# Performance work log

Hardware: AMD Instinct MI355X
Metric: run time of the kernel (lower is better)

## Reference

```python
import jax, jax.numpy as jnp
import numpy as np

HEADS = 8

def _conv1x1(x, W, b):
    # x: [n, Cin, H, W]; W: [Cout, Cin]; b: [Cout]
    return jnp.einsum('nchw,oc->nohw', x, W) + b[None, :, None, None]

def setup_inputs() -> dict:
    key = jax.random.key(0)
    ks = jax.random.split(key, 11)
    n, Cin, H, W = 8, 256, 80, 80
    Ck, Cv = 256, 256
    s_in = 1.0 / np.sqrt(Cin)
    s_v = 1.0 / np.sqrt(Cv)
    return {
        'query_feature': jax.random.normal(ks[0], (n, Cin, H, W), jnp.float32),
        'key_feature': jax.random.normal(ks[1], (n, Cin, H, W), jnp.float32),
        'value_feature': jax.random.normal(ks[2], (n, Cin, H, W), jnp.float32),
        'Wq': jax.random.normal(ks[3], (Ck, Cin), jnp.float32) * s_in,
        'bq': jax.random.normal(ks[4], (Ck,), jnp.float32) * s_in,
        'Wk': jax.random.normal(ks[5], (Ck, Cin), jnp.float32) * s_in,
        'bk': jax.random.normal(ks[6], (Ck,), jnp.float32) * s_in,
        'Wv': jax.random.normal(ks[7], (Cv, Cin), jnp.float32) * s_in,
        'bv': jax.random.normal(ks[8], (Cv,), jnp.float32) * s_in,
        'Wr': jax.random.normal(ks[9], (Cin, Cv), jnp.float32) * s_v,
        'br': jax.random.normal(ks[10], (Cin,), jnp.float32) * s_v,
    }

def reference(query_feature, key_feature, value_feature, Wq, bq, Wk, bk, Wv, bv, Wr, br):
    n, _, qh, qw = query_feature.shape
    kvn, _, kvh, kvw = key_feature.shape
    Ck = Wq.shape[0]
    Cv = Wv.shape[0]
    hk = Ck // HEADS
    hv = Cv // HEADS
    Lq = qh * qw
    Lkv = kvh * kvw
    # 1x1 conv projections, split channels into heads (consecutive channel blocks)
    q = _conv1x1(query_feature, Wq, bq).reshape(n, HEADS, hk, Lq)
    k = _conv1x1(key_feature, Wk, bk).reshape(kvn, HEADS, hk, Lkv)
    v = _conv1x1(value_feature, Wv, bv).reshape(kvn, HEADS, hv, Lkv)
    # softmax: keys over spatial positions, queries over head channels
    k = jax.nn.softmax(k, axis=3)
    q = jax.nn.softmax(q, axis=2)
    # efficient (linear) attention: context = K @ V^T, out = context^T @ Q
    context = jnp.einsum('nhkl,nhvl->nhkv', k, v)          # [n, H, hk, hv]
    attended = jnp.einsum('nhkv,nhkl->nhvl', context, q)   # [n, H, hv, Lq]
    aggregated = attended.reshape(n, Cv, qh, qw)
    return _conv1x1(aggregated, Wr, br) + query_feature
```

## Files before the change

### kernel.cpp

```cpp
#include <hip/hip_runtime.h>
#include <hip/hip_bf16.h>

#define NB 8
#define C 256
#define LL 6400
#define HEADS 8
#define HC 32
#define NH 64
#define SEG 40
#define SL 160
#define QPP 264
#define XTP 264

typedef unsigned short u16;
typedef unsigned int u32;
typedef __attribute__((ext_vector_type(8))) short bf16x8;
typedef __attribute__((ext_vector_type(4))) float f32x4;

typedef __attribute__((address_space(1))) const u32 ga_u32;
typedef __attribute__((address_space(3))) u32 ls_u32;

__device__ __forceinline__ void gload_lds16(const u16* g, u16* l) {
  __builtin_amdgcn_global_load_lds((ga_u32*)g, (ls_u32*)l, 16, 0, 0);
}

__device__ __forceinline__ float bf2f(u32 u) { return __uint_as_float(u << 16); }
__device__ __forceinline__ u16 f2bf(float f) {
  __hip_bfloat16 h = __float2bfloat16(f);
  return *(u16*)&h;
}
__device__ __forceinline__ void unpack8(uint4 u, float* f) {
  f[0] = bf2f(u.x & 0xffffu); f[1] = bf2f(u.x >> 16);
  f[2] = bf2f(u.y & 0xffffu); f[3] = bf2f(u.y >> 16);
  f[4] = bf2f(u.z & 0xffffu); f[5] = bf2f(u.z >> 16);
  f[6] = bf2f(u.w & 0xffffu); f[7] = bf2f(u.w >> 16);
}

struct WcvtArgs { const float* W[3]; u16* Wb[3]; };
struct PFArgs { const float* X[3]; const u16* Wb[3]; const float* bias[3]; u16* P[3]; };

__global__ __launch_bounds__(256) void wcvt(WcvtArgs a) {
  const int idx = blockIdx.x * 256 + threadIdx.x;
  const int which = idx >> 14, off = (idx & 16383) * 4;
  float4 v = *(const float4*)&a.W[which][off];
  ushort4 o = {f2bf(v.x), f2bf(v.y), f2bf(v.z), f2bf(v.w)};
  *(ushort4*)&a.Wb[which][off] = o;
}

__global__ __launch_bounds__(256, 2) void proj_fused(PFArgs args) {
  __shared__ __align__(16) u16 Xt[64 * XTP];
  __shared__ __align__(16) u16 Bs[2][256 * 32];
  const int which = blockIdx.y >> 3, n = blockIdx.y & 7;
  const int l0 = blockIdx.x * 64;
  const int t = threadIdx.x;
  const int lane = t & 63, wave = t >> 6;
  const int fr = lane & 15, q = lane >> 4;
  const int wl = (wave & 1) * 32, wco = (wave >> 1) * 128;
  const int s16 = t & 15, rc16 = t >> 4;
  const int srow = t >> 2, scol = (t & 3) * 8;
  const float* X = args.X[which] + (size_t)n * C * LL;
  const u16* Wb = args.Wb[which];

#pragma unroll
  for (int s = 0; s < 4; ++s)
    gload_lds16(&Wb[(size_t)(s * 64 + srow) * C + scol], &Bs[0][s * 2048 + wave * 512]);

  float4 xv[16];
#pragma unroll
  for (int cc = 0; cc < 16; ++cc)
    xv[cc] = *(const float4*)&X[(size_t)(rc16 * 16 + cc) * LL + l0 + s16 * 4];
#pragma unroll
  for (int j = 0; j < 4; ++j) {
    const int l = s16 * 4 + j;
    u32 w[8];
#pragma unroll
    for (int p = 0; p < 8; ++p) {
      const float* e0 = (const float*)&xv[2 * p];
      const float* e1 = (const float*)&xv[2 * p + 1];
      w[p] = (u32)f2bf(e0[j]) | ((u32)f2bf(e1[j]) << 16);
    }
    const int base = l * XTP + rc16 * 16;
    const int sw = (l & 7) << 3;
    uint4 lo = {w[0], w[1], w[2], w[3]};
    uint4 hi = {w[4], w[5], w[6], w[7]};
    *(uint4*)&Xt[(base) ^ sw] = lo;
    *(uint4*)&Xt[(base + 8) ^ sw] = hi;
  }
  __syncthreads();

  f32x4 acc[2][8] = {};
#pragma unroll
  for (int kt = 0; kt < 8; ++kt) {
    if (kt < 7) {
#pragma unroll
      for (int s = 0; s < 4; ++s)
        gload_lds16(&Wb[(size_t)(s * 64 + srow) * C + (kt + 1) * 32 + scol],
                    &Bs[(kt + 1) & 1][s * 2048 + wave * 512]);
    }
    bf16x8 a[2];
#pragma unroll
    for (int i = 0; i < 2; ++i) {
      const int row = wl + i * 16 + fr;
      a[i] = *(const bf16x8*)&Xt[(row * XTP + kt * 32 + q * 8) ^ ((row & 7) << 3)];
    }
#pragma unroll
    for (int j = 0; j < 8; ++j) {
      bf16x8 b = *(const bf16x8*)&Bs[kt & 1][(wco + j * 16 + fr) * 32 + q * 8];
#pragma unroll
      for (int i = 0; i < 2; ++i)
        acc[i][j] = __builtin_amdgcn_mfma_f32_16x16x32_bf16(a[i], b, acc[i][j], 0, 0, 0);
    }
    __syncthreads();
  }

  const float* bias = args.bias[which];
  u16* P = args.P[which] + (size_t)n * LL * C;
  float bb[8];
#pragma unroll
  for (int j = 0; j < 8; ++j) bb[j] = bias[wco + j * 16 + fr];
#pragma unroll
  for (int i = 0; i < 2; ++i)
#pragma unroll
    for (int r = 0; r < 4; ++r) {
      const int lrow = wl + i * 16 + q * 4 + r;
#pragma unroll
      for (int j = 0; j < 8; ++j)
        Xt[lrow * XTP + wco + j * 16 + fr] = f2bf(acc[i][j][r] + bb[j]);
    }
  __syncthreads();
  const int rg = t >> 5, ch = t & 31;
#pragma unroll
  for (int s = 0; s < 8; ++s) {
    const int row = rg * 8 + s;
    bf16x8 vrow = *(const bf16x8*)&Xt[row * XTP + ch * 8];
    *(bf16x8*)&P[(size_t)(l0 + row) * C + ch * 8] = vrow;
  }
}

__global__ __launch_bounds__(256) void ctx_part(const u16* __restrict__ Kt,
    const u16* __restrict__ Vt, float* __restrict__ pctx, float* __restrict__ psum) {
  __shared__ __align__(16) u16 Ks[16 * 256];
  __shared__ __align__(16) u16 Vs[16 * 256];
  const int seg = blockIdx.x, n = blockIdx.y;
  const int t = threadIdx.x, lane = t & 63, wave = t >> 6;
  const int l0 = seg * SL;
  const u16* KtN = Kt + (size_t)n * LL * C;
  const u16* VtN = Vt + (size_t)n * LL * C;
  const int k4 = (lane & 7) * 4, v8 = lane >> 3;
  float acc[2][4][4] = {};
  float ssum[2][4] = {};
  for (int ls = 0; ls < SL; ls += 16) {
    __syncthreads();
#pragma unroll
    for (int i = 0; i < 2; ++i) {
      const int r = wave * 4 + i * 2;
      gload_lds16(&KtN[(size_t)(l0 + ls + r) * C + lane * 8], &Ks[r * 256]);
      gload_lds16(&VtN[(size_t)(l0 + ls + r) * C + lane * 8], &Vs[r * 256]);
    }
    __syncthreads();
#pragma unroll
    for (int hh = 0; hh < 2; ++hh) {
      const int h = wave * 2 + hh;
#pragma unroll
      for (int l = 0; l < 16; ++l) {
        ushort4 ku = *(const ushort4*)&Ks[l * 256 + h * 32 + k4];
        ushort4 vu = *(const ushort4*)&Vs[l * 256 + h * 32 + v8 * 4];
        float ek[4] = {__expf(bf2f(ku.x)), __expf(bf2f(ku.y)),
                       __expf(bf2f(ku.z)), __expf(bf2f(ku.w))};
        float vf[4] = {bf2f(vu.x), bf2f(vu.y), bf2f(vu.z), bf2f(vu.w)};
#pragma unroll
        for (int i = 0; i < 4; ++i)
#pragma unroll
          for (int j = 0; j < 4; ++j) acc[hh][i][j] = fmaf(ek[i], vf[j], acc[hh][i][j]);
        if (v8 == 0)
#pragma unroll
          for (int i = 0; i < 4; ++i) ssum[hh][i] += ek[i];
      }
    }
  }
#pragma unroll
  for (int hh = 0; hh < 2; ++hh) {
    const int h = wave * 2 + hh;
    const size_t pb = ((size_t)seg * NH + n * 8 + h) * 1024;
#pragma unroll
    for (int i = 0; i < 4; ++i)
#pragma unroll
      for (int j = 0; j < 4; ++j)
        pctx[pb + (size_t)(k4 + i) * 32 + v8 * 4 + j] = acc[hh][i][j];
    if (v8 == 0) {
      const size_t sb = ((size_t)seg * NH + n * 8 + h) * 32;
#pragma unroll
      for (int i = 0; i < 4; ++i) psum[sb + k4 + i] = ssum[hh][i];
    }
  }
}

__global__ __launch_bounds__(256) void ctx_reduce(const float* __restrict__ pctx,
    const float* __restrict__ psum, float* __restrict__ ctx) {
  const int idx = blockIdx.x * 256 + threadIdx.x;
  const int nh = idx >> 10, e = idx & 1023, k = e >> 5;
  float s = 0.f, ss = 0.f;
  for (int g = 0; g < SEG; ++g) {
    s += pctx[(size_t)(g * NH + nh) * 1024 + e];
    ss += psum[(size_t)(g * NH + nh) * 32 + k];
  }
  ctx[idx] = s / ss;
}

__global__ __launch_bounds__(256) void mfuse(const float* __restrict__ Wr,
    const float* __restrict__ ctx, u16* __restrict__ M) {
  const int idx = blockIdx.x * 256 + threadIdx.x;
  const int hk = idx & 255;
  const int o = (idx >> 8) & 255;
  const int n = idx >> 16;
  const int h = hk >> 5, k = hk & 31;
  const float* wr = Wr + (size_t)o * C + h * HC;
  const float* cx = ctx + ((size_t)(n * HEADS + h) * HC + k) * HC;
  float s = 0.f;
#pragma unroll
  for (int v = 0; v < HC; ++v) s = fmaf(wr[v], cx[v], s);
  M[idx] = f2bf(s);
}

__global__ __launch_bounds__(256) void out_fused(const u16* __restrict__ Qt,
    const u16* __restrict__ Mb, const float* __restrict__ br,
    const float* __restrict__ Xq, float* __restrict__ out) {
  __shared__ __align__(16) u16 Qp[64 * QPP];
  __shared__ __align__(16) u16 As[2][128 * 32];
  const int n = blockIdx.y, l0 = blockIdx.x * 64;
  const int t = threadIdx.x, lane = t & 63, wave = t >> 6;
  const int fr = lane & 15, q = lane >> 4;
  const int wcoL = (wave >> 1) * 64, wl = (wave & 1) * 32;
  const int srow = t >> 2, scol = (t & 3) * 8;
  const u16* QtN = Qt + (size_t)n * LL * C;
  const u16* MbN = Mb + (size_t)n * C * C;

#pragma unroll
  for (int s = 0; s < 2; ++s)
    gload_lds16(&MbN[(size_t)(s * 64 + srow) * C + scol], &As[0][s * 2048 + wave * 512]);

#pragma unroll
  for (int p = 0; p < 2; ++p) {
    const int row = p * 32 + (t >> 3);
    const int g = t & 7;
    const uint4* src = (const uint4*)&QtN[(size_t)(l0 + row) * C + g * 32];
    uint4 u0 = src[0], u1 = src[1], u2 = src[2], u3 = src[3];
    float v[32];
    unpack8(u0, v); unpack8(u1, v + 8); unpack8(u2, v + 16); unpack8(u3, v + 24);
    float e[32], s = 0.f;
#pragma unroll
    for (int j = 0; j < 32; ++j) { e[j] = __expf(v[j]); s += e[j]; }
    const float r = 1.0f / s;
    uint4* drow = (uint4*)&Qp[row * QPP + g * 32];
#pragma unroll
    for (int b4 = 0; b4 < 4; ++b4) {
      union { uint4 u; u16 h[8]; } o;
#pragma unroll
      for (int j = 0; j < 8; ++j) o.h[j] = f2bf(e[b4 * 8 + j] * r);
      drow[b4] = o.u;
    }
  }
  asm volatile("s_waitcnt vmcnt(0) lgkmcnt(0)" ::: "memory");
  __builtin_amdgcn_s_barrier();
  __builtin_amdgcn_sched_barrier(0);

  f32x4 acc[2][4][2] = {};
#pragma unroll
  for (int it = 0; it < 16; ++it) {
    const int coh = it >> 3, k0 = (it & 7) * 32, cur = it & 1;
    if (it < 15) {
      const int nco = (it + 1) >> 3, nk0 = ((it + 1) & 7) * 32;
#pragma unroll
      for (int s = 0; s < 2; ++s)
        gload_lds16(&MbN[(size_t)(nco * 128 + s * 64 + srow) * C + nk0 + scol],
                    &As[cur ^ 1][s * 2048 + wave * 512]);
      __builtin_amdgcn_sched_barrier(0);
    }
    bf16x8 a[4], b[2];
#pragma unroll
    for (int i = 0; i < 4; ++i)
      a[i] = *(const bf16x8*)&As[cur][(wcoL + i * 16 + fr) * 32 + q * 8];
#pragma unroll
    for (int j = 0; j < 2; ++j)
      b[j] = *(const bf16x8*)&Qp[(wl + j * 16 + fr) * QPP + k0 + q * 8];
#pragma unroll
    for (int i = 0; i < 4; ++i)
#pragma unroll
      for (int j = 0; j < 2; ++j)
        acc[coh][i][j] = __builtin_amdgcn_mfma_f32_16x16x32_bf16(a[i], b[j], acc[coh][i][j], 0, 0, 0);
    if (it < 15) {
      asm volatile("s_waitcnt vmcnt(0) lgkmcnt(0)" ::: "memory");
      __builtin_amdgcn_s_barrier();
      __builtin_amdgcn_sched_barrier(0);
    }
  }

  const float* XqN = Xq + (size_t)n * C * LL;
  float* On = out + (size_t)n * C * LL;
#pragma unroll
  for (int coh = 0; coh < 2; ++coh)
#pragma unroll
    for (int i = 0; i < 4; ++i)
#pragma unroll
      for (int r = 0; r < 4; ++r) {
        const int co = coh * 128 + wcoL + i * 16 + q * 4 + r;
        const float bb = br[co];
#pragma unroll
        for (int j = 0; j < 2; ++j) {
          const int l = l0 + wl + j * 16 + fr;
          const size_t off = (size_t)co * LL + l;
          On[off] = acc[coh][i][j][r] + bb + XqN[off];
        }
      }
}

extern "C" void kernel_launch(void* const* d_in, const int* in_sizes, int n_in,
                              void* d_out, int out_size, void* d_ws, size_t ws_size,
                              hipStream_t stream) {
  const float* Xq = (const float*)d_in[0];
  const float* Xk = (const float*)d_in[1];
  const float* Xv = (const float*)d_in[2];
  const float* Wq = (const float*)d_in[3];
  const float* bq = (const float*)d_in[4];
  const float* Wk = (const float*)d_in[5];
  const float* bk = (const float*)d_in[6];
  const float* Wv = (const float*)d_in[7];
  const float* bv = (const float*)d_in[8];
  const float* Wr = (const float*)d_in[9];
  const float* br = (const float*)d_in[10];
  float* out = (float*)d_out;

  char* ws = (char*)d_ws;
  const size_t nelem = (size_t)NB * LL * C;
  u16* Qt = (u16*)ws;
  u16* Kt = (u16*)(ws + nelem * 2);
  u16* Vt = (u16*)(ws + nelem * 4);
  char* p = ws + nelem * 6;
  u16* Wqb = (u16*)p; p += C * C * 2;
  u16* Wkb = (u16*)p; p += C * C * 2;
  u16* Wvb = (u16*)p; p += C * C * 2;
  float* pctx = (float*)p; p += (size_t)SEG * NH * HC * HC * 4;
  float* psum = (float*)p; p += (size_t)SEG * NH * HC * 4;
  float* ctx = (float*)p;  p += (size_t)NH * HC * HC * 4;
  u16* Mb = (u16*)p;

  WcvtArgs wa;
  wa.W[0] = Wq; wa.W[1] = Wk; wa.W[2] = Wv;
  wa.Wb[0] = Wqb; wa.Wb[1] = Wkb; wa.Wb[2] = Wvb;
  wcvt<<<192, 256, 0, stream>>>(wa);

  PFArgs pa;
  pa.X[0] = Xq; pa.X[1] = Xk; pa.X[2] = Xv;
  pa.Wb[0] = Wqb; pa.Wb[1] = Wkb; pa.Wb[2] = Wvb;
  pa.bias[0] = bq; pa.bias[1] = bk; pa.bias[2] = bv;
  pa.P[0] = Qt; pa.P[1] = Kt; pa.P[2] = Vt;
  proj_fused<<<dim3(100, 24), 256, 0, stream>>>(pa);

  ctx_part<<<dim3(SEG, NB), 256, 0, stream>>>(Kt, Vt, pctx, psum);
  ctx_reduce<<<NH * HC * HC / 256, 256, 0, stream>>>(pctx, psum, ctx);
  mfuse<<<NB * C * C / 256, 256, 0, stream>>>(Wr, ctx, Mb);
  out_fused<<<dim3(100, NB), 256, 0, stream>>>(Qt, Mb, br, Xq, out);
}
```

Measured before the change: 333.5 us.

## Split input fp32→bf16 transpose into separate kernel and swizzle weight layout

Adds an xcvt kernel that converts each fp32 input to bf16 and transposes it into the L-major workspace buffers, using a tile in shared memory and an XOR-swizzled channel order. proj_fused then streams these bf16 rows straight into LDS with async global_load_lds instead of doing strided fp32 loads and in-register conversion. It writes its projection output in place over the same buffers. The weight conversion kernel also pre-swizzles the bf16 weights so B-fragment LDS reads avoid bank conflicts. The cost is an extra bf16 write and read pass over all three inputs and one more kernel launch.

New measurement: 380.1 us. +14.0%, slower.

```diff
diff --git a/kernel.cpp b/kernel.cpp
--- a/kernel.cpp
+++ b/kernel.cpp
@@ -10,7 +10,6 @@
 #define SEG 40
 #define SL 160
 #define QPP 264
-#define XTP 264
 
 typedef unsigned short u16;
 typedef unsigned int u32;
@@ -37,18 +36,55 @@
 }
 
 struct WcvtArgs { const float* W[3]; u16* Wb[3]; };
-struct PFArgs { const float* X[3]; const u16* Wb[3]; const float* bias[3]; u16* P[3]; };
+struct XcvtArgs { const float* X[3]; u16* Xb[3]; };
+struct PFArgs { const u16* Xb[3]; const u16* Wb[3]; const float* bias[3]; u16* P[3]; };
 
 __global__ __launch_bounds__(256) void wcvt(WcvtArgs a) {
   const int idx = blockIdx.x * 256 + threadIdx.x;
-  const int which = idx >> 14, off = (idx & 16383) * 4;
-  float4 v = *(const float4*)&a.W[which][off];
-  ushort4 o = {f2bf(v.x), f2bf(v.y), f2bf(v.z), f2bf(v.w)};
-  *(ushort4*)&a.Wb[which][off] = o;
+  const int which = idx >> 13, r = idx & 8191;
+  const int co = r >> 5, c8 = r & 31;
+  const float* src = a.W[which] + co * 256 + c8 * 8;
+  float4 v0 = *(const float4*)src, v1 = *(const float4*)(src + 4);
+  union { bf16x8 v; u16 h[8]; } o;
+  o.h[0] = f2bf(v0.x); o.h[1] = f2bf(v0.y); o.h[2] = f2bf(v0.z); o.h[3] = f2bf(v0.w);
+  o.h[4] = f2bf(v1.x); o.h[5] = f2bf(v1.y); o.h[6] = f2bf(v1.z); o.h[7] = f2bf(v1.w);
+  const int p = (c8 & ~3) | ((c8 & 3) ^ ((co >> 1) & 3));
+  *(bf16x8*)&a.Wb[which][co * 256 + p * 8] = o.v;
+}
+
+__global__ __launch_bounds__(256) void xcvt(XcvtArgs a) {
+  __shared__ float tile[64][68];
+  const int l0 = blockIdx.x * 64;
+  const int ct = blockIdx.y;
+  const int pz = blockIdx.z;
+  const int which = pz >> 3, n = pz & 7;
+  const int t = threadIdx.x;
+  const float* X = a.X[which] + (size_t)n * C * LL;
+  const int cr = t >> 2, lq = t & 3;
+#pragma unroll
+  for (int p = 0; p < 4; ++p) {
+    float4 v = *(const float4*)&X[(size_t)(ct * 64 + cr) * LL + l0 + (lq * 4 + p) * 4];
+    *(float4*)&tile[cr][(lq * 4 + p) * 4] = v;
+  }
+  __syncthreads();
+  u16* Xb = a.Xb[which] + (size_t)n * LL * C;
+  const int u3 = t & 7;
+#pragma unroll
+  for (int w2 = 0; w2 < 2; ++w2) {
+    const int lc = (t >> 3) + w2 * 32;
+    union { bf16x8 v; u16 h[8]; } o;
+#pragma unroll
+    for (int e = 0; e < 8; ++e) {
+      const int ep = e ^ u3;
+      o.h[ep] = f2bf(tile[u3 * 8 + ep][lc]);
+    }
+    const int p3 = u3 ^ (lc & 7);
+    *(bf16x8*)&Xb[(size_t)(l0 + lc) * C + (ct * 8 + p3) * 8] = o.v;
+  }
 }
 
 __global__ __launch_bounds__(256, 2) void proj_fused(PFArgs args) {
-  __shared__ __align__(16) u16 Xt[64 * XTP];
+  __shared__ __align__(16) u16 Xp[64 * 256];
   __shared__ __align__(16) u16 Bs[2][256 * 32];
   const int which = blockIdx.y >> 3, n = blockIdx.y & 7;
   const int l0 = blockIdx.x * 64;
@@ -56,39 +92,22 @@
   const int lane = t & 63, wave = t >> 6;
   const int fr = lane & 15, q = lane >> 4;
   const int wl = (wave & 1) * 32, wco = (wave >> 1) * 128;
-  const int s16 = t & 15, rc16 = t >> 4;
   const int srow = t >> 2, scol = (t & 3) * 8;
-  const float* X = args.X[which] + (size_t)n * C * LL;
+  const u16* Xb = args.Xb[which] + (size_t)n * LL * C;
   const u16* Wb = args.Wb[which];
 
+#pragma unroll
+  for (int s = 0; s < 8; ++s) {
+    const int rp = wave * 8 + s;
+    gload_lds16(&Xb[(size_t)(l0 + rp * 2) * C + lane * 8], &Xp[rp * 512]);
+  }
 #pragma unroll
   for (int s = 0; s < 4; ++s)
     gload_lds16(&Wb[(size_t)(s * 64 + srow) * C + scol], &Bs[0][s * 2048 + wave * 512]);
-
-  float4 xv[16];
-#pragma unroll
-  for (int cc = 0; cc < 16; ++cc)
-    xv[cc] = *(const float4*)&X[(size_t)(rc16 * 16 + cc) * LL + l0 + s16 * 4];
-#pragma unroll
-  for (int j = 0; j < 4; ++j) {
-    const int l = s16 * 4 + j;
-    u32 w[8];
-#pragma unroll
-    for (int p = 0; p < 8; ++p) {
-      const float* e0 = (const float*)&xv[2 * p];
-      const float* e1 = (const float*)&xv[2 * p + 1];
-      w[p] = (u32)f2bf(e0[j]) | ((u32)f2bf(e1[j]) << 16);
-    }
-    const int base = l * XTP + rc16 * 16;
-    const int sw = (l & 7) << 3;
-    uint4 lo = {w[0], w[1], w[2], w[3]};
-    uint4 hi = {w[4], w[5], w[6], w[7]};
-    *(uint4*)&Xt[(base) ^ sw] = lo;
-    *(uint4*)&Xt[(base + 8) ^ sw] = hi;
-  }
   __syncthreads();
 
   f32x4 acc[2][8] = {};
+  const int sco = (fr >> 1) & 3;
 #pragma unroll
   for (int kt = 0; kt < 8; ++kt) {
     if (kt < 7) {
@@ -101,11 +120,11 @@
 #pragma unroll
     for (int i = 0; i < 2; ++i) {
       const int row = wl + i * 16 + fr;
-      a[i] = *(const bf16x8*)&Xt[(row * XTP + kt * 32 + q * 8) ^ ((row & 7) << 3)];
+      a[i] = *(const bf16x8*)&Xp[row * 256 + (((kt * 4 + q) ^ (row & 7)) * 8)];
     }
 #pragma unroll
     for (int j = 0; j < 8; ++j) {
-      bf16x8 b = *(const bf16x8*)&Bs[kt & 1][(wco + j * 16 + fr) * 32 + q * 8];
+      bf16x8 b = *(const bf16x8*)&Bs[kt & 1][(wco + j * 16 + fr) * 32 + ((q ^ sco) * 8)];
 #pragma unroll
       for (int i = 0; i < 2; ++i)
         acc[i][j] = __builtin_amdgcn_mfma_f32_16x16x32_bf16(a[i], b, acc[i][j], 0, 0, 0);
@@ -125,14 +144,14 @@
       const int lrow = wl + i * 16 + q * 4 + r;
 #pragma unroll
       for (int j = 0; j < 8; ++j)
-        Xt[lrow * XTP + wco + j * 16 + fr] = f2bf(acc[i][j][r] + bb[j]);
+        Xp[lrow * 256 + wco + j * 16 + fr] = f2bf(acc[i][j][r] + bb[j]);
     }
   __syncthreads();
   const int rg = t >> 5, ch = t & 31;
 #pragma unroll
   for (int s = 0; s < 8; ++s) {
     const int row = rg * 8 + s;
-    bf16x8 vrow = *(const bf16x8*)&Xt[row * XTP + ch * 8];
+    bf16x8 vrow = *(const bf16x8*)&Xp[row * 256 + ch * 8];
     *(bf16x8*)&P[(size_t)(l0 + row) * C + ch * 8] = vrow;
   }
 }
@@ -347,10 +366,15 @@
   WcvtArgs wa;
   wa.W[0] = Wq; wa.W[1] = Wk; wa.W[2] = Wv;
   wa.Wb[0] = Wqb; wa.Wb[1] = Wkb; wa.Wb[2] = Wvb;
-  wcvt<<<192, 256, 0, stream>>>(wa);
+  wcvt<<<96, 256, 0, stream>>>(wa);
+
+  XcvtArgs xa;
+  xa.X[0] = Xq; xa.X[1] = Xk; xa.X[2] = Xv;
+  xa.Xb[0] = Qt; xa.Xb[1] = Kt; xa.Xb[2] = Vt;
+  xcvt<<<dim3(100, 4, 24), 256, 0, stream>>>(xa);
 
   PFArgs pa;
-  pa.X[0] = Xq; pa.X[1] = Xk; pa.X[2] = Xv;
+  pa.Xb[0] = Qt; pa.Xb[1] = Kt; pa.Xb[2] = Vt;
   pa.Wb[0] = Wqb; pa.Wb[1] = Wkb; pa.Wb[2] = Wvb;
   pa.bias[0] = bq; pa.bias[1] = bk; pa.bias[2] = bv;
   pa.P[0] = Qt; pa.P[1] = Kt; pa.P[2] = Vt;
```
